# Performance work log

Measured on AMD Instinct MI355X. Metric: run time of the kernel, lower is better.

## Reference

```python
import jax, jax.numpy as jnp
import numpy as np

H, W = 2048, 2048
T_MAX = 30.0
P_MAX = 1.0
# (di, dj, dist_coeff) for the 8-neighborhood, diagonals weighted 0.83
OFFSETS = [(-1, -1, 0.83), (-1, 0, 1.0), (-1, 1, 0.83),
           (0, -1, 1.0),               (0, 1, 1.0),
           (1, -1, 0.83), (1, 0, 1.0), (1, 1, 0.83)]


def _shift(x, di, dj):
    """shifted[i,j] = x[i+di, j+dj], zero outside the grid.
    Equivalent to the torch clamp-index + validity-mask gather, since the mask
    zeroes every out-of-range contribution."""
    p = jnp.pad(x, ((1, 1), (1, 1)))
    return p[1 + di:1 + di + x.shape[0], 1 + dj:1 + dj + x.shape[1]]


def setup_inputs() -> dict:
    key = jax.random.key(0)
    k_h, k_a, k_m, k_w = jax.random.split(key, 4)
    return {
        "log_alpha": jnp.zeros((), jnp.float32),   # log(1.0)
        "log_beta": jnp.zeros((), jnp.float32),
        "log_gamma": jnp.zeros((), jnp.float32),
        "height": jax.random.normal(k_h, (H, W), jnp.float32),
        "age": jax.random.uniform(k_a, (H, W), jnp.float32),
        "moisture": jax.random.uniform(k_m, (H, W), jnp.float32),
        "wind_grid": jax.random.uniform(k_w, (H, W), jnp.float32),
        "ignition_value": jnp.ones((), jnp.float32),
        "i0": 1024,
        "j0": 1024,
        "n_steps": 20,
        "n_substeps": 1,
    }


def _forward(log_alpha, log_beta, log_gamma, height, age, moisture,
             wind_grid, ignition_value, i0, j0, n_steps, n_substeps):
    alpha = jnp.exp(log_alpha)
    beta = jnp.exp(log_beta)
    gamma = jnp.exp(log_gamma)

    # age inflammability: (1+P_MAX)**((age/T_MAX)**alpha) - 1, saturating at P_MAX
    ratio = age / T_MAX
    below = (1.0 + P_MAX) ** (ratio ** alpha) - 1.0
    age_factor = jnp.where(age < T_MAX, below, P_MAX)
    psi = jnp.exp(-beta * moisture)
    gain = age_factor * psi                      # state-independent, hoisted

    # Precompute per-offset coefficient: dist * phi(dh) * validity_mask.
    valid = jnp.ones_like(height)
    coefs = []
    for di, dj, dist in OFFSETS:
        h_nb = _shift(height, di, dj)
        mask = _shift(valid, di, dj)             # 1 where neighbor in-grid
        dh = height - h_nb
        dh_safe = jnp.where(dh > 0, dh, 1.0)     # avoid sqrt'(0) = inf in grads
        downhill = jnp.exp(gamma * dh)
        uphill = 1.0 + gamma * jnp.sqrt(dh_safe)
        phi = jnp.where(dh <= 0, downhill, uphill)
        coefs.append(dist * phi * mask)

    def substep(state):
        ws = state * wind_grid                   # w_nb * s_nb share the shift
        total = jnp.zeros_like(state)
        for (di, dj, _), c in zip(OFFSETS, coefs):
            total = total + c * _shift(ws, di, dj)
        return jnp.clip(state + gain * total, 0.0, 1.0)

    state0 = jnp.zeros((H, W), height.dtype).at[i0, j0].set(ignition_value)
    arrival0 = jnp.full((H, W), float(n_steps), height.dtype)

    def body(carry, t):
        state, prev, arrival = carry
        for _ in range(n_substeps):              # static, typically 1
            state = substep(state)
        first_ignition = jnp.maximum(state - prev, 0.0)
        arrival = arrival - first_ignition * (float(n_steps) - t)
        prev = jax.lax.stop_gradient(state)      # mirrors state.detach()
        return (state, prev, arrival), None

    ts = jnp.arange(1, n_steps + 1, dtype=height.dtype)
    (_, _, arrival), _ = jax.lax.scan(body, (state0, jnp.zeros_like(state0), arrival0), ts)
    return arrival


def reference(log_alpha, log_beta, log_gamma, height, age, moisture,
              wind_grid, ignition_value, i0, j0, n_steps, n_substeps):
    return _forward(log_alpha, log_beta, log_gamma, height, age, moisture,
                    wind_grid, ignition_value, i0, j0, n_steps, n_substeps)
```

## Files before the change

kernel.cpp:

```cpp
#include <hip/hip_runtime.h>


namespace {
constexpr int H = 2048;
constexpr int W = 2048;
constexpr float T_MAX = 30.0f;
constexpr int WIN = 48;
constexpr int PH  = WIN + 2;
constexpr int PW  = WIN + 4;
constexpr int NT  = 576;
}

typedef float vfloat8 __attribute__((ext_vector_type(8)));

__global__ __launch_bounds__(NT, 1) void softfire_fused(
    const float* __restrict__ la_p, const float* __restrict__ lb_p,
    const float* __restrict__ lg_p, const float* __restrict__ height,
    const float* __restrict__ age, const float* __restrict__ moisture,
    const float* __restrict__ wind, const float* __restrict__ ign_p,
    const int* __restrict__ i0_p, const int* __restrict__ j0_p,
    const int* __restrict__ ns_p, const int* __restrict__ nsub_p,
    float* __restrict__ out)
{
    const int i0 = i0_p[0], j0 = j0_p[0];
    const int n_steps = ns_p[0];

    int bi = i0 - WIN / 2;
    bi = bi < 0 ? 0 : (bi > H - WIN ? H - WIN : bi);
    int bj = j0 - WIN / 2;
    bj = bj < 0 ? 0 : (bj > W - WIN ? W - WIN : bj);
    bj &= ~3;

    const int tid = threadIdx.x;

    if (blockIdx.x != 0) {
        const float v = (float)n_steps;
        const int idx = (int)(blockIdx.x - 1) * NT + tid;
        if (idx < (H * W) / 4) {
            const int row  = (idx * 4) / W;
            const int col4 = (idx * 4) % W;
            const bool inwin = (row >= bi) & (row < bi + WIN) &
                               (col4 >= bj) & (col4 < bj + WIN);
            if (!inwin)
                reinterpret_cast<float4*>(out)[idx] = make_float4(v, v, v, v);
        }
        return;
    }

    __shared__ float lds[4][PH * PW];

    const float alpha = expf(la_p[0]);
    const float beta  = expf(lb_p[0]);
    const float gamma = expf(lg_p[0]);
    const float ign   = ign_p[0];
    const int n_sub   = nsub_p[0];

    for (int k = tid; k < PH * PH; k += NT) {
        const int pr = k / PH, pc = k % PH;
        const int gi = bi - 1 + pr, gj = bj - 1 + pc;
        const size_t g = (size_t)gi * W + gj;
        const bool ingrid = (gi >= 0) & (gi < H) & (gj >= 0) & (gj < W);
        lds[0][pr * PW + pc] = ingrid ? height[g] : 0.0f;
        const bool inter = (pr >= 1) & (pr <= WIN) & (pc >= 1) & (pc <= WIN);
        lds[1][pr * PW + pc] = inter ? wind[g] : 0.0f;
        if (inter) {
            lds[2][pr * PW + pc] = age[g];
            lds[3][pr * PW + pc] = moisture[g];
        }
    }
    __syncthreads();

    const int R0 = 2 * (tid / 24);
    const int C0 = 2 * (tid % 24);

    const int ir = i0 - bi, jc = j0 - bj;
    int dr = 0;
    if (R0 > ir) dr = R0 - ir; else if (ir > R0 + 1) dr = ir - (R0 + 1);
    int dc = 0;
    if (C0 > jc) dc = C0 - jc; else if (jc > C0 + 1) dc = jc - (C0 + 1);
    const int dmin = dr > dc ? dr : dc;
    const int total_sub = n_steps * n_sub;
    const bool ever_active = (dmin <= total_sub);

    auto make_cf = [&](int R, int C) -> vfloat8 {
        const int   DI[8] = {-1,-1,-1, 0, 0, 1, 1, 1};
        const int   DJ[8] = {-1, 0, 1,-1, 1,-1, 0, 1};
        const float DS[8] = {0.83f, 1.0f, 0.83f, 1.0f, 1.0f, 0.83f, 1.0f, 0.83f};
        const int ci = (1 + R) * PW + (1 + C);
        const float h = lds[0][ci];
        const float a = lds[2][ci];
        const float m = lds[3][ci];
        const float ratio = a * (1.0f / T_MAX);
        const float ra = exp2f(alpha * log2f(ratio));
        const float below = exp2f(ra) - 1.0f;
        const float age_factor = (a < T_MAX) ? below : 1.0f;
        const float gn = age_factor * expf(-beta * m);
        vfloat8 cf;
        #pragma unroll
        for (int k = 0; k < 8; ++k) {
            const int ni = ci + DI[k] * PW + DJ[k];
            const float hn = lds[0][ni];
            const float wn = lds[1][ni];
            const float dh = h - hn;
            const float phi = (dh <= 0.0f) ? expf(gamma * dh)
                                           : (1.0f + gamma * sqrtf(dh));
            cf[k] = gn * DS[k] * phi * wn;
        }
        return cf;
    };

    vfloat8 cfA = (vfloat8)0.0f, cfB = (vfloat8)0.0f,
            cfC = (vfloat8)0.0f, cfD = (vfloat8)0.0f;
    if (ever_active) {
        cfA = make_cf(R0,     C0);
        cfB = make_cf(R0,     C0 + 1);
        cfC = make_cf(R0 + 1, C0);
        cfD = make_cf(R0 + 1, C0 + 1);
    }

    float stA = 0.0f, stB = 0.0f, stC = 0.0f, stD = 0.0f;
    if (bi + R0 == i0     && bj + C0 == j0)     stA = ign;
    if (bi + R0 == i0     && bj + C0 + 1 == j0) stB = ign;
    if (bi + R0 + 1 == i0 && bj + C0 == j0)     stC = ign;
    if (bi + R0 + 1 == i0 && bj + C0 + 1 == j0) stD = ign;
    float pvA = 0.0f, pvB = 0.0f, pvC = 0.0f, pvD = 0.0f;
    float arA = (float)n_steps, arB = arA, arC = arA, arD = arA;

    __syncthreads();

    const int igk = (1 + ir) * PW + (1 + jc);
    for (int k = tid; k < PH * PW; k += NT) {
        lds[0][k] = (k == igk) ? ign : 0.0f;
        lds[1][k] = 0.0f;
    }
    __syncthreads();

    int sel = 0;
    int tg = 0;
    const int tl = R0 * PW + C0;
    for (int t = 1; t <= n_steps; ++t) {
      for (int s = 0; s < n_sub; ++s) {
        ++tg;
        if (dmin <= tg) {
          const float* __restrict__ src = lds[sel];
          float* __restrict__ dst = lds[sel ^ 1];
          const float2* s2 = reinterpret_cast<const float2*>(src + tl);
          const float2 p00 = s2[0],          p01 = s2[1];
          const float2 p10 = s2[PW / 2],     p11 = s2[PW / 2 + 1];
          const float2 p20 = s2[PW],         p21 = s2[PW + 1];
          const float2 p30 = s2[3 * PW / 2], p31 = s2[3 * PW / 2 + 1];
          const float n00 = p00.x, n01 = p00.y, n02 = p01.x, n03 = p01.y;
          const float n10 = p10.x, n11 = p10.y, n12 = p11.x, n13 = p11.y;
          const float n20 = p20.x, n21 = p20.y, n22 = p21.x, n23 = p21.y;
          const float n30 = p30.x, n31 = p30.y, n32 = p31.x, n33 = p31.y;

#define FIRE_CELL(cf, a0, a1, a2, a3, a4, a5, a6, a7, ctr)                 \
          ({ float t0 = cf[0] * (a0), t1 = cf[1] * (a1);                   \
             t0 = fmaf(cf[2], (a2), t0); t1 = fmaf(cf[3], (a3), t1);       \
             t0 = fmaf(cf[4], (a4), t0); t1 = fmaf(cf[5], (a5), t1);       \
             t0 = fmaf(cf[6], (a6), t0); t1 = fmaf(cf[7], (a7), t1);       \
             fminf(fmaxf((ctr) + (t0 + t1), 0.0f), 1.0f); })

          stA = FIRE_CELL(cfA, n00, n01, n02, n10, n12, n20, n21, n22, n11);
          stB = FIRE_CELL(cfB, n01, n02, n03, n11, n13, n21, n22, n23, n12);
          stC = FIRE_CELL(cfC, n10, n11, n12, n20, n22, n30, n31, n32, n21);
          stD = FIRE_CELL(cfD, n11, n12, n13, n21, n23, n31, n32, n33, n22);
#undef FIRE_CELL

          dst[tl + PW + 1]     = stA;
          dst[tl + PW + 2]     = stB;
          dst[tl + 2 * PW + 1] = stC;
          dst[tl + 2 * PW + 2] = stD;
        }
        __syncthreads();
        sel ^= 1;
      }
      if (dmin <= tg) {
        const float wgt = (float)(n_steps - t);
        arA -= fmaxf(stA - pvA, 0.0f) * wgt;  pvA = stA;
        arB -= fmaxf(stB - pvB, 0.0f) * wgt;  pvB = stB;
        arC -= fmaxf(stC - pvC, 0.0f) * wgt;  pvC = stC;
        arD -= fmaxf(stD - pvD, 0.0f) * wgt;  pvD = stD;
      }
    }

    float2* o0 = reinterpret_cast<float2*>(out + (size_t)(bi + R0) * W + (bj + C0));
    float2* o1 = reinterpret_cast<float2*>(out + (size_t)(bi + R0 + 1) * W + (bj + C0));
    o0[0] = make_float2(arA, arB);
    o1[0] = make_float2(arC, arD);
}

extern "C" void kernel_launch(void* const* d_in, const int* in_sizes, int n_in,
                              void* d_out, int out_size, void* d_ws, size_t ws_size,
                              hipStream_t stream) {
    const float* log_alpha = (const float*)d_in[0];
    const float* log_beta  = (const float*)d_in[1];
    const float* log_gamma = (const float*)d_in[2];
    const float* height    = (const float*)d_in[3];
    const float* age       = (const float*)d_in[4];
    const float* moisture  = (const float*)d_in[5];
    const float* wind      = (const float*)d_in[6];
    const float* ign       = (const float*)d_in[7];
    const int*   i0        = (const int*)d_in[8];
    const int*   j0        = (const int*)d_in[9];
    const int*   n_steps   = (const int*)d_in[10];
    const int*   n_sub     = (const int*)d_in[11];
    float* out = (float*)d_out;

    const int fill_blocks = (H * W / 4 + NT - 1) / NT;
    softfire_fused<<<fill_blocks + 1, NT, 0, stream>>>(
        log_alpha, log_beta, log_gamma, height, age, moisture, wind, ign,
        i0, j0, n_steps, n_sub, out);
}
```

Baseline: 131.4 us.

## Fuse two substeps per barrier via halo recompute with global coefficient table

The stencil loop now advances two substeps per __syncthreads. Each thread loads a 6x6 neighbourhood, recomputes the 12 surrounding halo cells for the intermediate step, and reads their coefficients from a workspace table in global memory that the threads write before the loop. The arrival-time accumulation is also rewritten as a running sum of states subtracted from n_steps, which removes the per-step prev/max bookkeeping. This halves the number of block barriers, at the cost of roughly four times the FMA work per pair and many global vector loads of coefficients inside the hot loop.

```diff
diff --git a/kernel.cpp b/kernel.cpp
--- a/kernel.cpp
+++ b/kernel.cpp
@@ -6,12 +6,21 @@
 constexpr int W = 2048;
 constexpr float T_MAX = 30.0f;
 constexpr int WIN = 48;
-constexpr int PH  = WIN + 2;
-constexpr int PW  = WIN + 4;
+constexpr int SH  = WIN + 4;
+constexpr int SWD = WIN + 6;
+constexpr int CT  = WIN + 2;
 constexpr int NT  = 576;
 }
 
 typedef float vfloat8 __attribute__((ext_vector_type(8)));
+
+#define CLIP01(x) fminf(fmaxf((x), 0.0f), 1.0f)
+#define STEP8(cf, nw, nn, ne, ww, ee, sw, ss, se, ctr)                     \
+    ({ float t0_ = cf[0] * (nw), t1_ = cf[1] * (nn);                       \
+       t0_ = fmaf(cf[2], (ne), t0_); t1_ = fmaf(cf[3], (ww), t1_);         \
+       t0_ = fmaf(cf[4], (ee), t0_); t1_ = fmaf(cf[5], (sw), t1_);         \
+       t0_ = fmaf(cf[6], (ss), t0_); t1_ = fmaf(cf[7], (se), t1_);         \
+       CLIP01((ctr) + (t0_ + t1_)); })
 
 __global__ __launch_bounds__(NT, 1) void softfire_fused(
     const float* __restrict__ la_p, const float* __restrict__ lb_p,
@@ -20,7 +29,7 @@
     const float* __restrict__ wind, const float* __restrict__ ign_p,
     const int* __restrict__ i0_p, const int* __restrict__ j0_p,
     const int* __restrict__ ns_p, const int* __restrict__ nsub_p,
-    float* __restrict__ out)
+    float* __restrict__ out, float* __restrict__ gtab)
 {
     const int i0 = i0_p[0], j0 = j0_p[0];
     const int n_steps = ns_p[0];
@@ -47,25 +56,28 @@
         return;
     }
 
-    __shared__ float lds[4][PH * PW];
+    __shared__ float sbuf[2][SH * SWD];
+    __shared__ float ast[WIN * WIN];
+    __shared__ float mst[WIN * WIN];
 
     const float alpha = expf(la_p[0]);
     const float beta  = expf(lb_p[0]);
     const float gamma = expf(lg_p[0]);
     const float ign   = ign_p[0];
     const int n_sub   = nsub_p[0];
-
-    for (int k = tid; k < PH * PH; k += NT) {
-        const int pr = k / PH, pc = k % PH;
+    const int total_sub = n_steps * n_sub;
+
+    for (int k = tid; k < CT * CT; k += NT) {
+        const int pr = k / CT, pc = k % CT;
         const int gi = bi - 1 + pr, gj = bj - 1 + pc;
         const size_t g = (size_t)gi * W + gj;
         const bool ingrid = (gi >= 0) & (gi < H) & (gj >= 0) & (gj < W);
-        lds[0][pr * PW + pc] = ingrid ? height[g] : 0.0f;
+        sbuf[0][(pr + 1) * SWD + (pc + 1)] = ingrid ? height[g] : 0.0f;
         const bool inter = (pr >= 1) & (pr <= WIN) & (pc >= 1) & (pc <= WIN);
-        lds[1][pr * PW + pc] = inter ? wind[g] : 0.0f;
+        sbuf[1][(pr + 1) * SWD + (pc + 1)] = inter ? wind[g] : 0.0f;
         if (inter) {
-            lds[2][pr * PW + pc] = age[g];
-            lds[3][pr * PW + pc] = moisture[g];
+            ast[(pr - 1) * WIN + (pc - 1)] = age[g];
+            mst[(pr - 1) * WIN + (pc - 1)] = moisture[g];
         }
     }
     __syncthreads();
@@ -79,17 +91,16 @@
     int dc = 0;
     if (C0 > jc) dc = C0 - jc; else if (jc > C0 + 1) dc = jc - (C0 + 1);
     const int dmin = dr > dc ? dr : dc;
-    const int total_sub = n_steps * n_sub;
-    const bool ever_active = (dmin <= total_sub);
+    const bool build = (dmin <= total_sub + 2);
 
     auto make_cf = [&](int R, int C) -> vfloat8 {
         const int   DI[8] = {-1,-1,-1, 0, 0, 1, 1, 1};
         const int   DJ[8] = {-1, 0, 1,-1, 1,-1, 0, 1};
         const float DS[8] = {0.83f, 1.0f, 0.83f, 1.0f, 1.0f, 0.83f, 1.0f, 0.83f};
-        const int ci = (1 + R) * PW + (1 + C);
-        const float h = lds[0][ci];
-        const float a = lds[2][ci];
-        const float m = lds[3][ci];
+        const int ci = (R + 2) * SWD + (C + 2);
+        const float h = sbuf[0][ci];
+        const float a = ast[R * WIN + C];
+        const float m = mst[R * WIN + C];
         const float ratio = a * (1.0f / T_MAX);
         const float ra = exp2f(alpha * log2f(ratio));
         const float below = exp2f(ra) - 1.0f;
@@ -98,9 +109,9 @@
         vfloat8 cf;
         #pragma unroll
         for (int k = 0; k < 8; ++k) {
-            const int ni = ci + DI[k] * PW + DJ[k];
-            const float hn = lds[0][ni];
-            const float wn = lds[1][ni];
+            const int ni = ci + DI[k] * SWD + DJ[k];
+            const float hn = sbuf[0][ni];
+            const float wn = sbuf[1][ni];
             const float dh = h - hn;
             const float phi = (dh <= 0.0f) ? expf(gamma * dh)
                                            : (1.0f + gamma * sqrtf(dh));
@@ -111,83 +122,113 @@
 
     vfloat8 cfA = (vfloat8)0.0f, cfB = (vfloat8)0.0f,
             cfC = (vfloat8)0.0f, cfD = (vfloat8)0.0f;
-    if (ever_active) {
+    if (build) {
         cfA = make_cf(R0,     C0);
         cfB = make_cf(R0,     C0 + 1);
         cfC = make_cf(R0 + 1, C0);
         cfD = make_cf(R0 + 1, C0 + 1);
-    }
-
-    float stA = 0.0f, stB = 0.0f, stC = 0.0f, stD = 0.0f;
-    if (bi + R0 == i0     && bj + C0 == j0)     stA = ign;
-    if (bi + R0 == i0     && bj + C0 + 1 == j0) stB = ign;
-    if (bi + R0 + 1 == i0 && bj + C0 == j0)     stC = ign;
-    if (bi + R0 + 1 == i0 && bj + C0 + 1 == j0) stD = ign;
-    float pvA = 0.0f, pvB = 0.0f, pvC = 0.0f, pvD = 0.0f;
-    float arA = (float)n_steps, arB = arA, arC = arA, arD = arA;
+        *(vfloat8*)(gtab + ((((R0 + 1) * CT) + (C0 + 1)) << 3)) = cfA;
+        *(vfloat8*)(gtab + ((((R0 + 1) * CT) + (C0 + 2)) << 3)) = cfB;
+        *(vfloat8*)(gtab + ((((R0 + 2) * CT) + (C0 + 1)) << 3)) = cfC;
+        *(vfloat8*)(gtab + ((((R0 + 2) * CT) + (C0 + 2)) << 3)) = cfD;
+    }
+    __threadfence_block();
 
     __syncthreads();
 
-    const int igk = (1 + ir) * PW + (1 + jc);
-    for (int k = tid; k < PH * PW; k += NT) {
-        lds[0][k] = (k == igk) ? ign : 0.0f;
-        lds[1][k] = 0.0f;
+    const int igk = (ir + 2) * SWD + (jc + 2);
+    for (int k = tid; k < SH * SWD; k += NT) {
+        sbuf[0][k] = (k == igk) ? ign : 0.0f;
+        sbuf[1][k] = 0.0f;
     }
     __syncthreads();
 
-    int sel = 0;
-    int tg = 0;
-    const int tl = R0 * PW + C0;
-    for (int t = 1; t <= n_steps; ++t) {
-      for (int s = 0; s < n_sub; ++s) {
-        ++tg;
-        if (dmin <= tg) {
-          const float* __restrict__ src = lds[sel];
-          float* __restrict__ dst = lds[sel ^ 1];
-          const float2* s2 = reinterpret_cast<const float2*>(src + tl);
-          const float2 p00 = s2[0],          p01 = s2[1];
-          const float2 p10 = s2[PW / 2],     p11 = s2[PW / 2 + 1];
-          const float2 p20 = s2[PW],         p21 = s2[PW + 1];
-          const float2 p30 = s2[3 * PW / 2], p31 = s2[3 * PW / 2 + 1];
-          const float n00 = p00.x, n01 = p00.y, n02 = p01.x, n03 = p01.y;
-          const float n10 = p10.x, n11 = p10.y, n12 = p11.x, n13 = p11.y;
-          const float n20 = p20.x, n21 = p20.y, n22 = p21.x, n23 = p21.y;
-          const float n30 = p30.x, n31 = p30.y, n32 = p31.x, n33 = p31.y;
-
-#define FIRE_CELL(cf, a0, a1, a2, a3, a4, a5, a6, a7, ctr)                 \
-          ({ float t0 = cf[0] * (a0), t1 = cf[1] * (a1);                   \
-             t0 = fmaf(cf[2], (a2), t0); t1 = fmaf(cf[3], (a3), t1);       \
-             t0 = fmaf(cf[4], (a4), t0); t1 = fmaf(cf[5], (a5), t1);       \
-             t0 = fmaf(cf[6], (a6), t0); t1 = fmaf(cf[7], (a7), t1);       \
-             fminf(fmaxf((ctr) + (t0 + t1), 0.0f), 1.0f); })
-
-          stA = FIRE_CELL(cfA, n00, n01, n02, n10, n12, n20, n21, n22, n11);
-          stB = FIRE_CELL(cfB, n01, n02, n03, n11, n13, n21, n22, n23, n12);
-          stC = FIRE_CELL(cfC, n10, n11, n12, n20, n22, n30, n31, n32, n21);
-          stD = FIRE_CELL(cfD, n11, n12, n13, n21, n23, n31, n32, n33, n22);
-#undef FIRE_CELL
-
-          dst[tl + PW + 1]     = stA;
-          dst[tl + PW + 2]     = stB;
-          dst[tl + 2 * PW + 1] = stC;
-          dst[tl + 2 * PW + 2] = stD;
+#define CFT(RR, CC) \
+    (*(const vfloat8*)(gtab + ((((R0 + (RR) + 1) * CT) + (C0 + (CC) + 1)) << 3)))
+#define LOADROW(r, A, B, C, D, E, F)                                        \
+    { const float2 p_ = s2[(r) * 27], q_ = s2[(r) * 27 + 1],                \
+                   r_ = s2[(r) * 27 + 2];                                   \
+      A = p_.x; B = p_.y; C = q_.x; D = q_.y; E = r_.x; F = r_.y; }
+
+    int sel = 0, tg = 0, sis = 0, step = 0;
+    float sA = 0.0f, sB = 0.0f, sC = 0.0f, sD = 0.0f;
+
+    while (tg < total_sub) {
+        const bool pair = (total_sub - tg) >= 2;
+        const int tg_end = tg + (pair ? 2 : 1);
+        float o1A = 0, o1B = 0, o1C = 0, o1D = 0;
+        float o2A = 0, o2B = 0, o2C = 0, o2D = 0;
+        const float* __restrict__ src = sbuf[sel];
+        float* __restrict__ dst = sbuf[sel ^ 1];
+
+        if (dmin <= tg_end) {
+            const float2* s2 = (const float2*)(src + R0 * SWD + C0);
+            float x00,x01,x02,x03,x04,x05, x10,x11,x12,x13,x14,x15;
+            float x20,x21,x22,x23,x24,x25, x30,x31,x32,x33,x34,x35;
+            float x40,x41,x42,x43,x44,x45, x50,x51,x52,x53,x54,x55;
+            LOADROW(0, x00,x01,x02,x03,x04,x05)
+            LOADROW(1, x10,x11,x12,x13,x14,x15)
+            LOADROW(2, x20,x21,x22,x23,x24,x25)
+            LOADROW(3, x30,x31,x32,x33,x34,x35)
+            LOADROW(4, x40,x41,x42,x43,x44,x45)
+            LOADROW(5, x50,x51,x52,x53,x54,x55)
+
+            o1A = STEP8(cfA, x11,x12,x13,x21,x23,x31,x32,x33, x22);
+            o1B = STEP8(cfB, x12,x13,x14,x22,x24,x32,x33,x34, x23);
+            o1C = STEP8(cfC, x21,x22,x23,x31,x33,x41,x42,x43, x32);
+            o1D = STEP8(cfD, x22,x23,x24,x32,x34,x42,x43,x44, x33);
+
+            const int wb = (R0 + 2) * SWD + (C0 + 2);
+            if (pair) {
+                vfloat8 q;
+                q = CFT(-1,-1); const float a00 = STEP8(q, x00,x01,x02,x10,x12,x20,x21,x22, x11);
+                q = CFT(-1, 0); const float a01 = STEP8(q, x01,x02,x03,x11,x13,x21,x22,x23, x12);
+                q = CFT(-1, 1); const float a02 = STEP8(q, x02,x03,x04,x12,x14,x22,x23,x24, x13);
+                q = CFT(-1, 2); const float a03 = STEP8(q, x03,x04,x05,x13,x15,x23,x24,x25, x14);
+                q = CFT( 0,-1); const float a10 = STEP8(q, x10,x11,x12,x20,x22,x30,x31,x32, x21);
+                q = CFT( 0, 2); const float a13 = STEP8(q, x13,x14,x15,x23,x25,x33,x34,x35, x24);
+                q = CFT( 1,-1); const float a20 = STEP8(q, x20,x21,x22,x30,x32,x40,x41,x42, x31);
+                q = CFT( 1, 2); const float a23 = STEP8(q, x23,x24,x25,x33,x35,x43,x44,x45, x34);
+                q = CFT( 2,-1); const float a30 = STEP8(q, x30,x31,x32,x40,x42,x50,x51,x52, x41);
+                q = CFT( 2, 0); const float a31 = STEP8(q, x31,x32,x33,x41,x43,x51,x52,x53, x42);
+                q = CFT( 2, 1); const float a32 = STEP8(q, x32,x33,x34,x42,x44,x52,x53,x54, x43);
+                q = CFT( 2, 2); const float a33 = STEP8(q, x33,x34,x35,x43,x45,x53,x54,x55, x44);
+                o2A = STEP8(cfA, a00, a01, a02, a10, o1B, a20, o1C, o1D, o1A);
+                o2B = STEP8(cfB, a01, a02, a03, o1A, a13, o1C, o1D, a23, o1B);
+                o2C = STEP8(cfC, a10, o1A, o1B, a20, o1D, a30, a31, a32, o1C);
+                o2D = STEP8(cfD, o1A, o1B, a13, o1C, a23, a31, a32, a33, o1D);
+                dst[wb]           = o2A;
+                dst[wb + 1]       = o2B;
+                dst[wb + SWD]     = o2C;
+                dst[wb + SWD + 1] = o2D;
+            } else {
+                dst[wb]           = o1A;
+                dst[wb + 1]       = o1B;
+                dst[wb + SWD]     = o1C;
+                dst[wb + SWD + 1] = o1D;
+            }
         }
         __syncthreads();
         sel ^= 1;
-      }
-      if (dmin <= tg) {
-        const float wgt = (float)(n_steps - t);
-        arA -= fmaxf(stA - pvA, 0.0f) * wgt;  pvA = stA;
-        arB -= fmaxf(stB - pvB, 0.0f) * wgt;  pvB = stB;
-        arC -= fmaxf(stC - pvC, 0.0f) * wgt;  pvC = stC;
-        arD -= fmaxf(stD - pvD, 0.0f) * wgt;  pvD = stD;
-      }
-    }
-
+
+        if (++sis == n_sub) {
+            sis = 0; ++step;
+            if (step < n_steps) { sA += o1A; sB += o1B; sC += o1C; sD += o1D; }
+        }
+        if (pair) {
+            if (++sis == n_sub) {
+                sis = 0; ++step;
+                if (step < n_steps) { sA += o2A; sB += o2B; sC += o2C; sD += o2D; }
+            }
+        }
+        tg = tg_end;
+    }
+
+    const float T = (float)n_steps;
     float2* o0 = reinterpret_cast<float2*>(out + (size_t)(bi + R0) * W + (bj + C0));
     float2* o1 = reinterpret_cast<float2*>(out + (size_t)(bi + R0 + 1) * W + (bj + C0));
-    o0[0] = make_float2(arA, arB);
-    o1[0] = make_float2(arC, arD);
+    o0[0] = make_float2(T - sA, T - sB);
+    o1[0] = make_float2(T - sC, T - sD);
 }
 
 extern "C" void kernel_launch(void* const* d_in, const int* in_sizes, int n_in,
@@ -205,10 +246,11 @@
     const int*   j0        = (const int*)d_in[9];
     const int*   n_steps   = (const int*)d_in[10];
     const int*   n_sub     = (const int*)d_in[11];
-    float* out = (float*)d_out;
+    float* out  = (float*)d_out;
+    float* gtab = (float*)d_ws;
 
     const int fill_blocks = (H * W / 4 + NT - 1) / NT;
     softfire_fused<<<fill_blocks + 1, NT, 0, stream>>>(
         log_alpha, log_beta, log_gamma, height, age, moisture, wind, ign,
-        i0, j0, n_steps, n_sub, out);
+        i0, j0, n_steps, n_sub, out, gtab);
 }
```

Result: slower. 159.5 us (+21.4%).
